# Performance work log

Hardware: AMD Instinct MI355X
Metric: run time of the kernel (lower is better)

The kernel has to match this reference:

```python
import jax, jax.numpy as jnp
import numpy as np
from jax import lax

H, P, N, G, K, CHUNK = 64, 64, 128, 1, 4, 256
D_MODEL = 2048
D_INNER = H * P            # 4096
CONV_DIM = D_INNER + 2 * G * N  # 4352
EPS = 1e-5


def setup_inputs() -> dict:
    key = jax.random.key(0)
    ks = jax.random.split(key, 6)
    s = lambda k, shape, scale: jax.random.normal(k, shape, jnp.float32) * scale
    return {
        "hidden_states": s(ks[0], (2, 2048, D_MODEL), 1.0),
        "in_proj_w": s(ks[1], (D_MODEL, D_INNER + CONV_DIM + H), D_MODEL ** -0.5),
        "conv_w": s(ks[2], (CONV_DIM, K), K ** -0.5),
        "conv_b": jnp.zeros((CONV_DIM,), jnp.float32),
        "dt_bias": jnp.ones((H,), jnp.float32),
        "A_log": jnp.log(jnp.arange(1, H + 1, dtype=jnp.float32)),
        "D_param": jnp.ones((H,), jnp.float32),
        "norm_w": jnp.ones((D_INNER,), jnp.float32),
        "out_proj_w": s(ks[3], (D_INNER, D_MODEL), D_INNER ** -0.5),
    }


def _mamba2_forward(hidden_states, in_proj_w, conv_w, conv_b, dt_bias, A_log, D_param, norm_w, out_proj_w):
    b, l, _ = hidden_states.shape
    c = l // CHUNK  # number of chunks

    # in_proj -> gate | conv channels (x,B,C) | dt
    proj = hidden_states @ in_proj_w
    gate = proj[..., :D_INNER]
    hbc = proj[..., D_INNER:D_INNER + CONV_DIM]
    dt = proj[..., D_INNER + CONV_DIM:]  # [b,l,H]

    # depthwise causal conv1d + silu
    xt = hbc.transpose(0, 2, 1)  # [b, CONV_DIM, l]
    y = lax.conv_general_dilated(
        xt, conv_w[:, None, :], window_strides=(1,), padding=[(K - 1, 0)],
        feature_group_count=CONV_DIM, dimension_numbers=("NCH", "OIH", "NCH"))
    hbc = jax.nn.silu(y + conv_b[None, :, None]).transpose(0, 2, 1)  # [b,l,CONV_DIM]

    # split into x / B / C per group (unflatten over groups as in torch code)
    per_g = D_INNER // G
    hg = hbc.reshape(b, l, G, per_g + 2 * N)
    x = hg[..., :per_g].reshape(b, l, H, P)                 # [b,l,h,p]
    Bm = hg[..., per_g:per_g + N]                            # [b,l,g,n]
    Cm = hg[..., per_g + N:]                                 # [b,l,g,n]
    hpg = H // G
    Bh = jnp.repeat(Bm, hpg, axis=2)                         # [b,l,h,n]
    Ch = jnp.repeat(Cm, hpg, axis=2)

    # dt: softplus(dt + bias), clamp per time_step_limit (0, inf)
    dt = jax.nn.softplus(dt + dt_bias)                       # [b,l,h]
    A = -jnp.exp(A_log)                                      # [h]

    # chunk the sequence
    x_c = x.reshape(b, c, CHUNK, H, P)
    B_c = Bh.reshape(b, c, CHUNK, H, N)
    C_c = Ch.reshape(b, c, CHUNK, H, N)
    dt_c = dt.reshape(b, c, CHUNK, H)

    dA = dt_c * A[None, None, None, :]                       # [b,c,L,h]
    cum = jnp.cumsum(dA, axis=2)                             # [b,c,L,h]

    # intra-chunk (diagonal block): decay[i,j] = exp(cum_i - cum_j), i>=j
    diff = cum[:, :, :, None, :] - cum[:, :, None, :, :]     # [b,c,i,j,h]
    i = jnp.arange(CHUNK)
    mask = i[:, None] >= i[None, :]
    decay = jnp.exp(jnp.where(mask[None, None, :, :, None], diff, -jnp.inf))
    scores = jnp.einsum("bcihn,bcjhn->bcijh", C_c, B_c) * decay * dt_c[:, :, None, :, :]
    Y_diag = jnp.einsum("bcijh,bcjhp->bcihp", scores, x_c)   # [b,c,L,h,p]

    # per-chunk final states
    decay_states = jnp.exp(cum[:, :, -1:, :] - cum)          # [b,c,L,h]
    states = jnp.einsum("bclh,bclhn,bclhp->bchpn", decay_states * dt_c, B_c, x_c)
    chunk_decay = jnp.exp(cum[:, :, -1, :])                  # [b,c,h]

    # inter-chunk recurrence over chunks
    def step(prev, inp):
        st, cd = inp  # [b,h,p,n], [b,h]
        new = cd[:, :, None, None] * prev + st
        return new, prev

    init = jnp.zeros((b, H, P, N), hidden_states.dtype)
    _, prev_states = lax.scan(step, init, (jnp.moveaxis(states, 1, 0), jnp.moveaxis(chunk_decay, 1, 0)))
    prev_states = jnp.moveaxis(prev_states, 0, 1)            # [b,c,h,p,n]

    state_decay_out = jnp.exp(cum)                           # [b,c,L,h]
    Y_off = jnp.einsum("bclhn,bchpn,bclh->bclhp", C_c, prev_states, state_decay_out)

    yh = (Y_diag + Y_off).reshape(b, l, H, P) + D_param[None, None, :, None] * x
    yr = yh.reshape(b, l, D_INNER)

    # gated RMSNorm
    hidden = yr * jax.nn.silu(gate)
    var = jnp.mean(hidden * hidden, axis=-1, keepdims=True)
    hidden = hidden * lax.rsqrt(var + EPS) * norm_w

    return hidden @ out_proj_w


def reference(hidden_states, in_proj_w, conv_w, conv_b, dt_bias, A_log, D_param, norm_w, out_proj_w):
    return _mamba2_forward(hidden_states, in_proj_w, conv_w, conv_b, dt_bias, A_log, D_param, norm_w, out_proj_w)
```

## Files before the change

kernel.cpp:

```cpp
#include <hip/hip_runtime.h>
#include <hip/hip_bf16.h>


typedef __attribute__((ext_vector_type(8))) _Float16 f16x8;
typedef __attribute__((ext_vector_type(4))) float f32x4;

#define GLD16(gp, lp) __builtin_amdgcn_global_load_lds( \
    (__attribute__((address_space(1))) void*)(gp),      \
    (__attribute__((address_space(3))) void*)(lp), 16, 0, 0)

__device__ __forceinline__ unsigned short f2h(float v) {
  _Float16 h = (_Float16)v;
  return *reinterpret_cast<unsigned short*>(&h);
}
__device__ __forceinline__ float h2f(unsigned short u) {
  _Float16 h = *reinterpret_cast<_Float16*>(&u);
  return (float)h;
}
__device__ __forceinline__ float siluf(float x) { return x / (1.f + expf(-x)); }

__global__ __launch_bounds__(256) void prep(const float* __restrict__ hs,
                                            const float* __restrict__ Win,
                                            _Float16* __restrict__ Ah,
                                            _Float16* __restrict__ WtH,
                                            float* __restrict__ zf) {
  __shared__ __attribute__((aligned(16))) char smemP[32768];
  const int bid = blockIdx.x;
  const int tid = threadIdx.x;
  if (bid < 1024) {
    float (*Xs)[2048] = reinterpret_cast<float (*)[2048]>(smemP);
    int t0 = bid * 4;
#pragma unroll
    for (int i = 0; i < 8; i++) {
      int e = tid * 4 + i * 1024;
      int tok = e >> 11, k = e & 2047;
      *reinterpret_cast<float4*>(&Xs[tok][k]) =
          *reinterpret_cast<const float4*>(&hs[(long)(t0 + tok) * 2048 + k]);
    }
    __syncthreads();
    int h = tid & 63, tg = tid >> 6;
    float a0 = 0.f, a1 = 0.f, a2 = 0.f, a3 = 0.f;
    const float* wcol = Win + 8448 + h;
    for (int k = 0; k < 2048; k += 4) {
      a0 = fmaf(Xs[tg][k + 0], wcol[(long)(k + 0) * 8512], a0);
      a1 = fmaf(Xs[tg][k + 1], wcol[(long)(k + 1) * 8512], a1);
      a2 = fmaf(Xs[tg][k + 2], wcol[(long)(k + 2) * 8512], a2);
      a3 = fmaf(Xs[tg][k + 3], wcol[(long)(k + 3) * 8512], a3);
    }
    zf[(long)(t0 + tg) * 64 + h] = (a0 + a1) + (a2 + a3);
  } else if (bid < 9216) {
    long i = ((long)(bid - 1024) * 256 + tid) * 4;
    float4 v = *reinterpret_cast<const float4*>(hs + i);
    ushort4 u;
    u.x = f2h(v.x); u.y = f2h(v.y); u.z = f2h(v.z); u.w = f2h(v.w);
    *reinterpret_cast<ushort4*>((unsigned short*)Ah + i) = u;
  } else {
    float (*tile)[33] = reinterpret_cast<float (*)[33]>(smemP);
    int i = bid - 9216;
    int c0 = (i % 264) * 32, r0 = (i / 264) * 32;
    int tx = tid & 31, ty = tid >> 5;
#pragma unroll
    for (int j = 0; j < 4; j++)
      tile[ty + j * 8][tx] = Win[(long)(r0 + ty + j * 8) * 8512 + c0 + tx];
    __syncthreads();
#pragma unroll
    for (int j = 0; j < 4; j++) {
      int c = c0 + ty + j * 8, r = r0 + tx;
      WtH[(long)c * 2048 + r] = (_Float16)tile[tx][ty + j * 8];
    }
  }
}

__global__ __launch_bounds__(512, 2) void gemm_in8(const _Float16* __restrict__ A,
                                                   const _Float16* __restrict__ Bt,
                                                   _Float16* __restrict__ gate,
                                                   float* __restrict__ hbcf,
                                                   float* __restrict__ rparts) {
  __shared__ __attribute__((aligned(128))) char ldsB[131072];
  const int tid = threadIdx.x;
  const int lane = tid & 63;
  const int wv = tid >> 6;
  const int wr = wv >> 2, wc = wv & 3;
  const int wg = blockIdx.x;
  const bool rem = wg >= 512;
  int by, bxn, kbase, zz;
  if (!rem) {
    const int xcd = wg & 7, j = wg >> 3;
    by = (xcd >> 2) * 8 + (j >> 3);
    bxn = (xcd & 3) * 8 + (j & 7);
    kbase = 0; zz = 0;
  } else {
    const int idx = wg - 512;
    by = idx & 15; zz = idx >> 4; bxn = 32; kbase = zz * 256;
  }

  const int srow = tid >> 3;
  const int scolg = (tid & 7) ^ (srow & 7);
  const _Float16* Ab = A + (long)by * 524288 + (long)srow * 2048 + scolg * 8 + kbase;
  const _Float16* Bb = Bt + (long)bxn * 524288 + (long)srow * 2048 + scolg * 8 + kbase;
  const int ldst = tid << 4;

#define STAGE_A(tau, h) do {                                              \
    const _Float16* g_ = Ab + (long)(h) * 262144 + (tau) * 64;            \
    char* l_ = ldsB + ((((tau) & 1) << 2) + (h)) * 16384 + ldst;          \
    GLD16(g_, l_); GLD16(g_ + 131072, l_ + 8192); } while (0)
#define STAGE_B(tau, h) do {                                              \
    const _Float16* g_ = Bb + (long)(h) * 262144 + (tau) * 64;            \
    char* l_ = ldsB + ((((tau) & 1) << 2) + 2 + (h)) * 16384 + ldst;      \
    GLD16(g_, l_); GLD16(g_ + 131072, l_ + 8192); } while (0)

  const int fr = lane & 15;
  const int c16 = (lane >> 4) ^ (fr & 7);
  const int aOff = wr * 16384 + fr * 128 + c16 * 16;
  const int bOff = (2 + (wc >> 1)) * 16384 + ((wc & 1) * 64 + fr) * 128 + c16 * 16;
#define RD_A(b, mi, k32) (*(const f16x8*)(ldsB + ((aOff + (b) * 65536 + (mi) * 2048) ^ ((k32) * 64))))
#define RD_B(b, ni, k32) (*(const f16x8*)(ldsB + ((bOff + (b) * 65536 + (ni) * 2048) ^ ((k32) * 64))))

#define BAR() __builtin_amdgcn_s_barrier()
#define WLG0() asm volatile("s_waitcnt lgkmcnt(0)" ::: "memory")
#define WLG8() asm volatile("s_waitcnt lgkmcnt(8)" ::: "memory")
#define WVM4() asm volatile("s_waitcnt vmcnt(4)" ::: "memory")

  f32x4 acc[8][4];
#pragma unroll
  for (int mi = 0; mi < 8; ++mi)
#pragma unroll
    for (int ni = 0; ni < 4; ++ni) acc[mi][ni] = f32x4{0.f, 0.f, 0.f, 0.f};

  STAGE_A(0, 0); STAGE_A(0, 1); STAGE_B(0, 0); STAGE_B(0, 1);
  STAGE_B(1, 0); STAGE_B(1, 1);
  WVM4(); BAR();

#define MFMA_Q(MI0, MI1, x0, x1, x2, x3, PB)                                        \
  __builtin_amdgcn_s_setprio(1);                                                    \
  _Pragma("unroll") for (int ni = 0; ni < 4; ++ni) {                                \
    acc[MI0][ni] = __builtin_amdgcn_mfma_f32_16x16x32_f16(x0, PB[ni][0], acc[MI0][ni], 0, 0, 0); \
    acc[MI0][ni] = __builtin_amdgcn_mfma_f32_16x16x32_f16(x1, PB[ni][1], acc[MI0][ni], 0, 0, 0); \
    acc[MI1][ni] = __builtin_amdgcn_mfma_f32_16x16x32_f16(x2, PB[ni][0], acc[MI1][ni], 0, 0, 0); \
    acc[MI1][ni] = __builtin_amdgcn_mfma_f32_16x16x32_f16(x3, PB[ni][1], acc[MI1][ni], 0, 0, 0); \
  }                                                                                 \
  __builtin_amdgcn_s_setprio(0);

#define ITER8(u, msk) do {                                                          \
    const int t1 = (2 * (u) + 1) & (msk);                                           \
    const int t2 = (2 * (u) + 2) & (msk);                                           \
    const int t3 = (2 * (u) + 3) & (msk);                                           \
    f16x8 PB0[4][2];                                                                \
    _Pragma("unroll") for (int ni = 0; ni < 4; ++ni) {                              \
      PB0[ni][0] = RD_B(0, ni, 0); PB0[ni][1] = RD_B(0, ni, 1); }                   \
    {                                                                               \
      f16x8 x0 = RD_A(0, 0, 0), x1 = RD_A(0, 0, 1), x2 = RD_A(0, 1, 0), x3 = RD_A(0, 1, 1); \
      STAGE_A(t1, 0); WLG8(); BAR(); WLG0();                                        \
      MFMA_Q(0, 1, x0, x1, x2, x3, PB0) BAR();                                      \
    }                                                                               \
    {                                                                               \
      f16x8 x0 = RD_A(0, 2, 0), x1 = RD_A(0, 2, 1), x2 = RD_A(0, 3, 0), x3 = RD_A(0, 3, 1); \
      STAGE_A(t1, 1); BAR(); WLG0();                                                \
      MFMA_Q(2, 3, x0, x1, x2, x3, PB0) BAR();                                      \
    }                                                                               \
    {                                                                               \
      f16x8 x0 = RD_A(0, 4, 0), x1 = RD_A(0, 4, 1), x2 = RD_A(0, 5, 0), x3 = RD_A(0, 5, 1); \
      STAGE_B(t2, 0); BAR(); WLG0();                                                \
      MFMA_Q(4, 5, x0, x1, x2, x3, PB0) BAR();                                      \
    }                                                                               \
    {                                                                               \
      f16x8 x0 = RD_A(0, 6, 0), x1 = RD_A(0, 6, 1), x2 = RD_A(0, 7, 0), x3 = RD_A(0, 7, 1); \
      STAGE_B(t2, 1); BAR(); WLG0();                                                \
      MFMA_Q(6, 7, x0, x1, x2, x3, PB0) WVM4(); BAR();                              \
    }                                                                               \
    f16x8 PB1[4][2];                                                                \
    _Pragma("unroll") for (int ni = 0; ni < 4; ++ni) {                              \
      PB1[ni][0] = RD_B(1, ni, 0); PB1[ni][1] = RD_B(1, ni, 1); }                   \
    {                                                                               \
      f16x8 x0 = RD_A(1, 0, 0), x1 = RD_A(1, 0, 1), x2 = RD_A(1, 1, 0), x3 = RD_A(1, 1, 1); \
      STAGE_A(t2, 0); WLG8(); BAR(); WLG0();                                        \
      MFMA_Q(0, 1, x0, x1, x2, x3, PB1) BAR();                                      \
    }                                                                               \
    {                                                                               \
      f16x8 x0 = RD_A(1, 2, 0), x1 = RD_A(1, 2, 1), x2 = RD_A(1, 3, 0), x3 = RD_A(1, 3, 1); \
      STAGE_A(t2, 1); BAR(); WLG0();                                                \
      MFMA_Q(2, 3, x0, x1, x2, x3, PB1) BAR();                                      \
    }                                                                               \
    {                                                                               \
      f16x8 x0 = RD_A(1, 4, 0), x1 = RD_A(1, 4, 1), x2 = RD_A(1, 5, 0), x3 = RD_A(1, 5, 1); \
      STAGE_B(t3, 0); BAR(); WLG0();                                                \
      MFMA_Q(4, 5, x0, x1, x2, x3, PB1) BAR();                                      \
    }                                                                               \
    {                                                                               \
      f16x8 x0 = RD_A(1, 6, 0), x1 = RD_A(1, 6, 1), x2 = RD_A(1, 7, 0), x3 = RD_A(1, 7, 1); \
      STAGE_B(t3, 1); BAR(); WLG0();                                                \
      MFMA_Q(6, 7, x0, x1, x2, x3, PB1) WVM4(); BAR();                              \
    }                                                                               \
  } while (0)

  if (!rem) {
    for (int u = 0; u < 16; ++u) ITER8(u, 31);
  } else {
    for (int u = 0; u < 2; ++u) ITER8(u, 3);
  }

  const int m0 = by * 256 + wr * 128;
  const int cl = lane & 15, rq = (lane >> 4) * 4;
  if (!rem) {
    const int n0 = bxn * 256 + wc * 64;
    if (bxn < 16) {
#pragma unroll
      for (int mi = 0; mi < 8; ++mi)
#pragma unroll
        for (int r = 0; r < 4; ++r) {
          long rowoff = (long)(m0 + mi * 16 + rq + r) * 4096 + n0 + cl;
#pragma unroll
          for (int ni = 0; ni < 4; ++ni) gate[rowoff + ni * 16] = (_Float16)acc[mi][ni][r];
        }
    } else {
#pragma unroll
      for (int mi = 0; mi < 8; ++mi)
#pragma unroll
        for (int r = 0; r < 4; ++r) {
          long rowoff = (long)(m0 + mi * 16 + rq + r) * 4352 + (n0 - 4096) + cl;
#pragma unroll
          for (int ni = 0; ni < 4; ++ni) hbcf[rowoff + ni * 16] = acc[mi][ni][r];
        }
    }
  } else {
    float* rp = rparts + (long)zz * 1048576;
    const int ncol = wc * 64;
#pragma unroll
    for (int mi = 0; mi < 8; ++mi)
#pragma unroll
      for (int r = 0; r < 4; ++r) {
        long rowoff = (long)(m0 + mi * 16 + rq + r) * 256 + ncol + cl;
#pragma unroll
        for (int ni = 0; ni < 4; ++ni) rp[rowoff + ni * 16] = acc[mi][ni][r];
      }
  }
#undef STAGE_A
#undef STAGE_B
#undef RD_A
#undef RD_B
#undef ITER8
}

__global__ __launch_bounds__(256) void fuse2(const float* __restrict__ zf,
                                             const float* __restrict__ dtb,
                                             const float* __restrict__ Alog,
                                             float* __restrict__ dt_f,
                                             float* __restrict__ cum_f,
                                             float* __restrict__ cuml,
                                             const float* __restrict__ rp,
                                             float* __restrict__ hbcf,
                                             const float* __restrict__ Wout,
                                             _Float16* __restrict__ WoutT) {
  __shared__ __attribute__((aligned(16))) char smem2[4352];
  const int bid = blockIdx.x;
  const int tid = threadIdx.x;
  if (bid < 16) {
    float (*segsum)[64] = reinterpret_cast<float (*)[64]>(smem2);
    int bc = bid;
    int h = tid & 63, seg = tid >> 6;
    int t0 = bc * 256;
    float Ah = -expf(Alog[h]);
    float bias = dtb[h];
    float s = 0.f;
    for (int j = 0; j < 64; j++) {
      int t = t0 + seg * 64 + j;
      float z = zf[(long)t * 64 + h] + bias;
      float v = (z > 20.f) ? z : log1pf(expf(z));
      dt_f[(long)t * 64 + h] = v;
      s += v * Ah;
    }
    segsum[seg][h] = s;
    __syncthreads();
    float run = 0.f;
    for (int k = 0; k < seg; k++) run += segsum[k][h];
    for (int j = 0; j < 64; j++) {
      int t = t0 + seg * 64 + j;
      run += dt_f[(long)t * 64 + h] * Ah;
      cum_f[(long)t * 64 + h] = run;
    }
    if (seg == 3) cuml[bc * 64 + h] = run;
  } else if (bid < 1040) {
    long e = ((long)(bid - 16) * 256 + tid) * 4;
    float4 s = *reinterpret_cast<const float4*>(rp + e);
#pragma unroll
    for (int z = 1; z < 8; ++z) {
      float4 v = *reinterpret_cast<const float4*>(rp + (long)z * 1048576 + e);
      s.x += v.x; s.y += v.y; s.z += v.z; s.w += v.w;
    }
    long row = e >> 8, col = e & 255;
    *reinterpret_cast<float4*>(hbcf + row * 4352 + 4096 + col) = s;
  } else {
    float (*tile)[33] = reinterpret_cast<float (*)[33]>(smem2);
    int i = bid - 1040;
    int c0 = (i & 63) * 32, r0 = (i >> 6) * 32;
    int tx = tid & 31, ty = tid >> 5;
#pragma unroll
    for (int j = 0; j < 4; j++)
      tile[ty + j * 8][tx] = Wout[(long)(r0 + ty + j * 8) * 2048 + c0 + tx];
    __syncthreads();
#pragma unroll
    for (int j = 0; j < 4; j++) {
      int c = c0 + ty + j * 8, r = r0 + tx;
      WoutT[(long)c * 4096 + r] = (_Float16)tile[tx][ty + j * 8];
    }
  }
}

__global__ __launch_bounds__(256) void convx(const float* __restrict__ hbcf,
                                             const float* __restrict__ convw,
                                             const float* __restrict__ convb,
                                             _Float16* __restrict__ x16,
                                             _Float16* __restrict__ B16,
                                             _Float16* __restrict__ C16,
                                             unsigned short* __restrict__ xT16) {
  __shared__ unsigned short tile[64][66];
  const int bx = blockIdx.x, t0 = blockIdx.y * 64;
  const int tid = threadIdx.x;
  const int tq = tid & 63, tg = tid >> 6;
  const int q0 = (bx < 64) ? bx * 64 : 4096 + (bx - 64) * 64;
  const int q = q0 + tq;
  const int ts = t0 + tg * 16;
  const int bstart = ts & ~2047;
  const float* colq = hbcf + q;
  float4 wq = *reinterpret_cast<const float4*>(convw + q * 4);
  float bconv = convb[q];
  float v3 = (ts - 3 >= bstart) ? colq[(long)(ts - 3) * 4352] : 0.f;
  float v2 = (ts - 2 >= bstart) ? colq[(long)(ts - 2) * 4352] : 0.f;
  float v1 = (ts - 1 >= bstart) ? colq[(long)(ts - 1) * 4352] : 0.f;
  if (bx < 64) {
#pragma unroll
    for (int j = 0; j < 16; ++j) {
      int t = ts + j;
      float v0 = colq[(long)t * 4352];
      float a = bconv + v3 * wq.x + v2 * wq.y + v1 * wq.z + v0 * wq.w;
      unsigned short o = f2h(siluf(a));
      ((unsigned short*)x16)[(long)t * 4096 + q] = o;
      tile[tg * 16 + j][tq] = o;
      v3 = v2; v2 = v1; v1 = v0;
    }
    __syncthreads();
    int tx = tid & 15, ty = tid >> 4;
#pragma unroll
    for (int i = 0; i < 4; ++i) {
      int c = ty + i * 16;
      ushort4 v;
      v.x = tile[4 * tx + 0][c]; v.y = tile[4 * tx + 1][c];
      v.z = tile[4 * tx + 2][c]; v.w = tile[4 * tx + 3][c];
      *(ushort4*)&xT16[(long)(q0 + c) * 4096 + t0 + 4 * tx] = v;
    }
  } else {
#pragma unroll
    for (int j = 0; j < 16; ++j) {
      int t = ts + j;
      float v0 = colq[(long)t * 4352];
      float a = bconv + v3 * wq.x + v2 * wq.y + v1 * wq.z + v0 * wq.w;
      _Float16 o = (_Float16)siluf(a);
      if (q < 4224) B16[(long)t * 128 + (q - 4096)] = o;
      else C16[(long)t * 128 + (q - 4224)] = o;
      v3 = v2; v2 = v1; v1 = v0;
    }
  }
}

__global__ __launch_bounds__(256) void fuse3(const unsigned short* __restrict__ xT16,
                                             const _Float16* __restrict__ B16,
                                             const _Float16* __restrict__ C16,
                                             const float* __restrict__ dt_f,
                                             const float* __restrict__ cum_f,
                                             const float* __restrict__ cuml,
                                             float* __restrict__ states,
                                             float* __restrict__ CBT) {
  __shared__ __attribute__((aligned(16))) char smem3[16384];
  const int bid = blockIdx.x;
  const int tid = threadIdx.x;
  const int wv = tid >> 6, lane = tid & 63;
  const int mr = lane & 15, koff = (lane >> 4) * 8;
  if (bid < 1024) {
    float* w_s = (float*)smem3;
    unsigned short* Aw = (unsigned short*)(smem3 + 1024);
    unsigned short* BT = (unsigned short*)(smem3 + 6144);
    int h = bid & 63, bc = bid >> 6;
    int t0 = bc * 256;
    {
      int t = t0 + tid;
      w_s[tid] = expf(cuml[bc * 64 + h] - cum_f[(long)t * 64 + h]) * dt_f[(long)t * 64 + h];
    }
    __syncthreads();
    f32x4 acc[4][2];
#pragma unroll
    for (int mi = 0; mi < 4; mi++)
#pragma unroll
      for (int nj = 0; nj < 2; nj++) acc[mi][nj] = f32x4{0.f, 0.f, 0.f, 0.f};
    for (int kt = 0; kt < 8; kt++) {
      {
        int p = tid >> 2, tq2 = tid & 3;
        const unsigned short* g = &xT16[((long)(h * 64 + p)) * 4096 + t0 + kt * 32 + tq2 * 8];
        ushort4 u0 = *(const ushort4*)g, u1 = *(const ushort4*)(g + 4);
        const float* wp = &w_s[kt * 32 + tq2 * 8];
        ushort4 o0, o1;
        o0.x = f2h(h2f(u0.x) * wp[0]); o0.y = f2h(h2f(u0.y) * wp[1]);
        o0.z = f2h(h2f(u0.z) * wp[2]); o0.w = f2h(h2f(u0.w) * wp[3]);
        o1.x = f2h(h2f(u1.x) * wp[4]); o1.y = f2h(h2f(u1.y) * wp[5]);
        o1.z = f2h(h2f(u1.z) * wp[6]); o1.w = f2h(h2f(u1.w) * wp[7]);
        *(ushort4*)&Aw[p * 40 + tq2 * 8] = o0;
        *(ushort4*)&Aw[p * 40 + tq2 * 8 + 4] = o1;
      }
      {
        int tl = tid >> 3, ng = tid & 7;
        const unsigned short* g = (const unsigned short*)B16 +
                                  ((long)(t0 + kt * 32 + tl)) * 128 + ng * 16;
#pragma unroll
        for (int j = 0; j < 16; j++) BT[(ng * 16 + j) * 40 + tl] = g[j];
      }
      __syncthreads();
      f16x8 af[4], bf[2];
#pragma unroll
      for (int mi = 0; mi < 4; mi++)
        af[mi] = *(const f16x8*)&Aw[(mi * 16 + mr) * 40 + koff];
#pragma unroll
      for (int nj = 0; nj < 2; nj++)
        bf[nj] = *(const f16x8*)&BT[((wv * 2 + nj) * 16 + mr) * 40 + koff];
#pragma unroll
      for (int mi = 0; mi < 4; mi++)
#pragma unroll
        for (int nj = 0; nj < 2; nj++)
          acc[mi][nj] = __builtin_amdgcn_mfma_f32_16x16x32_f16(af[mi], bf[nj],
                                                               acc[mi][nj], 0, 0, 0);
      __syncthreads();
    }
    int cl = lane & 15, rq = (lane >> 4) * 4;
    long base = ((long)(bc * 64 + h)) * 8192;
#pragma unroll
    for (int mi = 0; mi < 4; mi++)
#pragma unroll
      for (int r = 0; r < 4; r++) {
        int p = mi * 16 + rq + r;
#pragma unroll
        for (int nj = 0; nj < 2; nj++) {
          int n = (wv * 2 + nj) * 16 + cl;
          states[base + p * 128 + n] = acc[mi][nj][r];
        }
      }
  } else {
    _Float16* As = (_Float16*)smem3;
    _Float16* Bs = (_Float16*)(smem3 + 8192);
    int i = bid - 1024;
    int bx = i & 1, by = (i >> 1) & 1, bz = i >> 2;
    const _Float16* Ab = C16 + (long)bz * 32768 + (long)by * 128 * 128;
    const _Float16* Bb = B16 + (long)bz * 32768 + (long)bx * 128 * 128;
    const int c0 = wv * 128 + lane;
    const int c1 = c0 + 64;
    const long ra0 = (long)(c0 >> 2) * 128 + (c0 & 3) * 8;
    const long ra1 = (long)(c1 >> 2) * 128 + (c1 & 3) * 8;
    f32x4 acc[4][4];
#pragma unroll
    for (int mi = 0; mi < 4; mi++)
#pragma unroll
      for (int ni = 0; ni < 4; ni++) acc[mi][ni] = f32x4{0.f, 0.f, 0.f, 0.f};
    const int mrow = (wv & 1) * 64 + (lane & 15);
    const int nrow = (wv >> 1) * 64 + (lane & 15);
    for (int k0 = 0; k0 < 128; k0 += 32) {
      GLD16(Ab + ra0 + k0, (char*)As + c0 * 16);
      GLD16(Ab + ra1 + k0, (char*)As + c1 * 16);
      GLD16(Bb + ra0 + k0, (char*)Bs + c0 * 16);
      GLD16(Bb + ra1 + k0, (char*)Bs + c1 * 16);
      __syncthreads();
      f16x8 af[4], bfr[4];
#pragma unroll
      for (int mi = 0; mi < 4; mi++)
        af[mi] = *(const f16x8*)(As + (mrow + mi * 16) * 32 + koff);
#pragma unroll
      for (int ni = 0; ni < 4; ni++)
        bfr[ni] = *(const f16x8*)(Bs + (nrow + ni * 16) * 32 + koff);
#pragma unroll
      for (int mi = 0; mi < 4; mi++)
#pragma unroll
        for (int ni = 0; ni < 4; ni++)
          acc[mi][ni] = __builtin_amdgcn_mfma_f32_16x16x32_f16(af[mi], bfr[ni],
                                                               acc[mi][ni], 0, 0, 0);
      __syncthreads();
    }
    const int m0 = by * 128 + (wv & 1) * 64;
    const int n0 = bx * 128 + (wv >> 1) * 64;
    const int cl = lane & 15, rq = (lane >> 4) * 4;
    const long zc = (long)bz * 65536;
#pragma unroll
    for (int mi = 0; mi < 4; mi++)
#pragma unroll
      for (int r = 0; r < 4; r++) {
        long rowoff = zc + (long)(m0 + mi * 16 + rq + r) * 256 + n0 + cl;
#pragma unroll
        for (int ni = 0; ni < 4; ni++) CBT[rowoff + ni * 16] = acc[mi][ni][r];
      }
  }
}

__global__ __launch_bounds__(256) void recur_kernel(float* __restrict__ states,
                                                    const float* __restrict__ cuml) {
  int g = blockIdx.x;
  int bh = g >> 3, js = g & 7;
  int b = bh >> 6, h = bh & 63;
  int tid = threadIdx.x;
  float4 prev = make_float4(0.f, 0.f, 0.f, 0.f);
  for (int c = 0; c < 8; c++) {
    int bc = b * 8 + c;
    float cd = expf(cuml[bc * 64 + h]);
    long o = (long)(bc * 64 + h) * 8192 + js * 1024 + tid * 4;
    float4 st = *reinterpret_cast<const float4*>(&states[o]);
    *reinterpret_cast<float4*>(&states[o]) = prev;
    prev.x = fmaf(cd, prev.x, st.x);
    prev.y = fmaf(cd, prev.y, st.y);
    prev.z = fmaf(cd, prev.z, st.z);
    prev.w = fmaf(cd, prev.w, st.w);
  }
}

__global__ __launch_bounds__(256) void yfused(const unsigned short* __restrict__ xT16,
                                              const unsigned short* __restrict__ x16,
                                              const unsigned short* __restrict__ C16,
                                              const float* __restrict__ CBT,
                                              const float* __restrict__ states,
                                              const float* __restrict__ dt_f,
                                              const float* __restrict__ cum_f,
                                              const float* __restrict__ Dp,
                                              float* __restrict__ Ysum) {
  int h = blockIdx.x, bc = blockIdx.y;
  int t0 = bc * 256, tid = threadIdx.x;
  __shared__ unsigned short Sb[256 * 40];
  __shared__ unsigned short Xb[64 * 264];
  __shared__ float cum_s[256], dt_s[256];
  int i = tid;
  cum_s[i] = cum_f[(long)(t0 + i) * 64 + h];
  dt_s[i] = dt_f[(long)(t0 + i) * 64 + h];
  {
    int p = tid >> 2, tq = tid & 3;
    const unsigned short* g = &xT16[((long)(h * 64 + p)) * 4096 + t0 + tq * 64];
    unsigned short* l = &Xb[p * 264 + tq * 64];
#pragma unroll
    for (int c = 0; c < 8; c++)
      *(uint4*)(l + c * 8) = *(const uint4*)(g + c * 8);
  }
  __syncthreads();
  float cum_i = cum_s[i];
  const float* cbrow = CBT + (long)bc * 65536 + (long)i * 256;
  int wv = tid >> 6, lane = tid & 63;
  int mr = lane & 15, koff = (lane >> 4) * 8;
  f32x4 acc[4][4];
#pragma unroll
  for (int mi = 0; mi < 4; mi++)
#pragma unroll
    for (int ni = 0; ni < 4; ni++) acc[mi][ni] = f32x4{0.f, 0.f, 0.f, 0.f};
  for (int kt = 0; kt < 8; kt++) {
    int k0 = kt * 32;
#pragma unroll
    for (int c = 0; c < 8; c++) {
      float4 cb = *(const float4*)&cbrow[k0 + c * 4];
      ushort4 o;
      {
        int j = k0 + c * 4 + 0;
        float s = (j <= i) ? cb.x * expf(cum_i - cum_s[j]) * dt_s[j] : 0.f;
        o.x = f2h(s);
      }
      {
        int j = k0 + c * 4 + 1;
        float s = (j <= i) ? cb.y * expf(cum_i - cum_s[j]) * dt_s[j] : 0.f;
        o.y = f2h(s);
      }
      {
        int j = k0 + c * 4 + 2;
        float s = (j <= i) ? cb.z * expf(cum_i - cum_s[j]) * dt_s[j] : 0.f;
        o.z = f2h(s);
      }
      {
        int j = k0 + c * 4 + 3;
        float s = (j <= i) ? cb.w * expf(cum_i - cum_s[j]) * dt_s[j] : 0.f;
        o.w = f2h(s);
      }
      *(ushort4*)&Sb[i * 40 + c * 4] = o;
    }
    __syncthreads();
    if (kt <= 2 * wv + 1) {
      f16x8 af[4], bf[4];
#pragma unroll
      for (int mi = 0; mi < 4; mi++)
        af[mi] = *(const f16x8*)&Sb[(64 * wv + mi * 16 + mr) * 40 + koff];
#pragma unroll
      for (int ni = 0; ni < 4; ni++)
        bf[ni] = *(const f16x8*)&Xb[(ni * 16 + mr) * 264 + k0 + koff];
#pragma unroll
      for (int mi = 0; mi < 4; mi++)
#pragma unroll
        for (int ni = 0; ni < 4; ni++)
          acc[mi][ni] = __builtin_amdgcn_mfma_f32_16x16x32_f16(af[mi], bf[ni],
                                                               acc[mi][ni], 0, 0, 0);
    }
    __syncthreads();
  }
  {
    int p = tid >> 2, nq = tid & 3;
    const float* g = &states[((long)(bc * 64 + h)) * 8192 + p * 128 + nq * 32];
    unsigned short* l = &Xb[p * 136 + nq * 32];
#pragma unroll
    for (int c = 0; c < 8; c++) {
      float4 v = *(const float4*)(g + c * 4);
      ushort4 u;
      u.x = f2h(v.x); u.y = f2h(v.y); u.z = f2h(v.z); u.w = f2h(v.w);
      *(ushort4*)(l + c * 4) = u;
    }
  }
  float fac_i = expf(cum_i);
  for (int kn = 0; kn < 4; kn++) {
    {
      const unsigned short* g = &C16[((long)(t0 + i)) * 128 + kn * 32];
#pragma unroll
      for (int c = 0; c < 8; c++) {
        ushort4 u = *(const ushort4*)(g + c * 4);
        ushort4 o;
        o.x = f2h(h2f(u.x) * fac_i); o.y = f2h(h2f(u.y) * fac_i);
        o.z = f2h(h2f(u.z) * fac_i); o.w = f2h(h2f(u.w) * fac_i);
        *(ushort4*)&Sb[i * 40 + c * 4] = o;
      }
    }
    __syncthreads();
    f16x8 af[4], bf[4];
#pragma unroll
    for (int mi = 0; mi < 4; mi++)
      af[mi] = *(const f16x8*)&Sb[(64 * wv + mi * 16 + mr) * 40 + koff];
#pragma unroll
    for (int ni = 0; ni < 4; ni++)
      bf[ni] = *(const f16x8*)&Xb[(ni * 16 + mr) * 136 + kn * 32 + koff];
#pragma unroll
    for (int mi = 0; mi < 4; mi++)
#pragma unroll
      for (int ni = 0; ni < 4; ni++)
        acc[mi][ni] = __builtin_amdgcn_mfma_f32_16x16x32_f16(af[mi], bf[ni],
                                                             acc[mi][ni], 0, 0, 0);
    __syncthreads();
  }
  float Dh = Dp[h];
  int cl = lane & 15, rq = (lane >> 4) * 4;
#pragma unroll
  for (int mi = 0; mi < 4; mi++)
#pragma unroll
    for (int r = 0; r < 4; r++) {
      long row = t0 + 64 * wv + mi * 16 + rq + r;
      float* yr = &Ysum[row * 4096 + h * 64];
      const unsigned short* xr = &x16[row * 4096 + h * 64];
#pragma unroll
      for (int ni = 0; ni < 4; ni++) {
        int p = ni * 16 + cl;
        yr[p] = acc[mi][ni][r] + Dh * h2f(xr[p]);
      }
    }
}

__global__ __launch_bounds__(256) void norm_kernel(const float* __restrict__ Ysum,
                                                   const _Float16* __restrict__ gate,
                                                   const float* __restrict__ nw,
                                                   _Float16* __restrict__ hid) {
  int t = blockIdx.x;
  int tid = threadIdx.x;
  float hv[16];
  float ss = 0.f;
#pragma unroll
  for (int k = 0; k < 4; k++) {
    int d = tid * 4 + k * 1024;
    float4 y = *reinterpret_cast<const float4*>(&Ysum[(long)t * 4096 + d]);
    ushort4 gu = *reinterpret_cast<const ushort4*>(gate + (long)t * 4096 + d);
    float h0 = y.x * siluf(h2f(gu.x)), h1 = y.y * siluf(h2f(gu.y));
    float h2 = y.z * siluf(h2f(gu.z)), h3 = y.w * siluf(h2f(gu.w));
    hv[k * 4 + 0] = h0; hv[k * 4 + 1] = h1; hv[k * 4 + 2] = h2; hv[k * 4 + 3] = h3;
    ss += h0 * h0 + h1 * h1 + h2 * h2 + h3 * h3;
  }
#pragma unroll
  for (int o = 32; o > 0; o >>= 1) ss += __shfl_down(ss, o, 64);
  __shared__ float ws4[4];
  if ((tid & 63) == 0) ws4[tid >> 6] = ss;
  __syncthreads();
  float var = (ws4[0] + ws4[1] + ws4[2] + ws4[3]) * (1.f / 4096.f);
  float scale = rsqrtf(var + 1e-5f);
#pragma unroll
  for (int k = 0; k < 4; k++) {
    int d = tid * 4 + k * 1024;
    ushort4 u;
#pragma unroll
    for (int c = 0; c < 4; c++)
      ((unsigned short*)&u)[c] = f2h(hv[k * 4 + c] * scale * nw[d + c]);
    *reinterpret_cast<ushort4*>(hid + (long)t * 4096 + d) = u;
  }
}

__global__ __launch_bounds__(512, 2) void gemm_out8(const _Float16* __restrict__ A,
                                                    const _Float16* __restrict__ Bt,
                                                    float* __restrict__ Cp) {
  __shared__ __attribute__((aligned(128))) char ldsB[131072];
  const int tid = threadIdx.x;
  const int lane = tid & 63;
  const int wv = tid >> 6;
  const int wr = wv >> 2, wc = wv & 3;
  const int wg = blockIdx.x;
  const int xcd = wg & 7, j = wg >> 3;
  const int z = j >> 4, t = j & 15;
  const int by = (xcd >> 1) * 4 + (t >> 2);
  const int bx = (xcd & 1) * 4 + (t & 3);

  const int srow = tid >> 3;
  const int scolg = (tid & 7) ^ (srow & 7);
  const _Float16* Ab = A + (long)by * 256 * 4096 + (long)z * 2048 +
                       (long)srow * 4096 + scolg * 8;
  const _Float16* Bb = Bt + (long)bx * 256 * 4096 + (long)z * 2048 +
                       (long)srow * 4096 + scolg * 8;
  const int ldst = tid << 4;

#define STAGE_A(tau, h) do {                                              \
    const _Float16* g_ = Ab + (long)(h) * 524288 + (tau) * 64;            \
    char* l_ = ldsB + ((((tau) & 1) << 2) + (h)) * 16384 + ldst;          \
    GLD16(g_, l_); GLD16(g_ + 262144, l_ + 8192); } while (0)
#define STAGE_B(tau, h) do {                                              \
    const _Float16* g_ = Bb + (long)(h) * 524288 + (tau) * 64;            \
    char* l_ = ldsB + ((((tau) & 1) << 2) + 2 + (h)) * 16384 + ldst;      \
    GLD16(g_, l_); GLD16(g_ + 262144, l_ + 8192); } while (0)

  const int fr = lane & 15;
  const int c16 = (lane >> 4) ^ (fr & 7);
  const int aOff = wr * 16384 + fr * 128 + c16 * 16;
  const int bOff = (2 + (wc >> 1)) * 16384 + ((wc & 1) * 64 + fr) * 128 + c16 * 16;
#define RD_A(b, mi, k32) (*(const f16x8*)(ldsB + ((aOff + (b) * 65536 + (mi) * 2048) ^ ((k32) * 64))))
#define RD_B(b, ni, k32) (*(const f16x8*)(ldsB + ((bOff + (b) * 65536 + (ni) * 2048) ^ ((k32) * 64))))

  f32x4 acc[8][4];
#pragma unroll
  for (int mi = 0; mi < 8; ++mi)
#pragma unroll
    for (int ni = 0; ni < 4; ++ni) acc[mi][ni] = f32x4{0.f, 0.f, 0.f, 0.f};

  STAGE_A(0, 0); STAGE_A(0, 1); STAGE_B(0, 0); STAGE_B(0, 1);
  STAGE_B(1, 0); STAGE_B(1, 1);
  WVM4(); BAR();

  for (int u = 0; u < 16; ++u) {
    const int t1 = 2 * u + 1;
    const int t2 = (2 * u + 2) & 31;
    const int t3 = (2 * u + 3) & 31;
    f16x8 PB0[4][2];
#pragma unroll
    for (int ni = 0; ni < 4; ++ni) { PB0[ni][0] = RD_B(0, ni, 0); PB0[ni][1] = RD_B(0, ni, 1); }
    {
      f16x8 x0 = RD_A(0, 0, 0), x1 = RD_A(0, 0, 1), x2 = RD_A(0, 1, 0), x3 = RD_A(0, 1, 1);
      STAGE_A(t1, 0); WLG8(); BAR(); WLG0();
      MFMA_Q(0, 1, x0, x1, x2, x3, PB0) BAR();
    }
    {
      f16x8 x0 = RD_A(0, 2, 0), x1 = RD_A(0, 2, 1), x2 = RD_A(0, 3, 0), x3 = RD_A(0, 3, 1);
      STAGE_A(t1, 1); BAR(); WLG0();
      MFMA_Q(2, 3, x0, x1, x2, x3, PB0) BAR();
    }
    {
      f16x8 x0 = RD_A(0, 4, 0), x1 = RD_A(0, 4, 1), x2 = RD_A(0, 5, 0), x3 = RD_A(0, 5, 1);
      STAGE_B(t2, 0); BAR(); WLG0();
      MFMA_Q(4, 5, x0, x1, x2, x3, PB0) BAR();
    }
    {
      f16x8 x0 = RD_A(0, 6, 0), x1 = RD_A(0, 6, 1), x2 = RD_A(0, 7, 0), x3 = RD_A(0, 7, 1);
      STAGE_B(t2, 1); BAR(); WLG0();
      MFMA_Q(6, 7, x0, x1, x2, x3, PB0) WVM4(); BAR();
    }
    f16x8 PB1[4][2];
#pragma unroll
    for (int ni = 0; ni < 4; ++ni) { PB1[ni][0] = RD_B(1, ni, 0); PB1[ni][1] = RD_B(1, ni, 1); }
    {
      f16x8 x0 = RD_A(1, 0, 0), x1 = RD_A(1, 0, 1), x2 = RD_A(1, 1, 0), x3 = RD_A(1, 1, 1);
      STAGE_A(t2, 0); WLG8(); BAR(); WLG0();
      MFMA_Q(0, 1, x0, x1, x2, x3, PB1) BAR();
    }
    {
      f16x8 x0 = RD_A(1, 2, 0), x1 = RD_A(1, 2, 1), x2 = RD_A(1, 3, 0), x3 = RD_A(1, 3, 1);
      STAGE_A(t2, 1); BAR(); WLG0();
      MFMA_Q(2, 3, x0, x1, x2, x3, PB1) BAR();
    }
    {
      f16x8 x0 = RD_A(1, 4, 0), x1 = RD_A(1, 4, 1), x2 = RD_A(1, 5, 0), x3 = RD_A(1, 5, 1);
      STAGE_B(t3, 0); BAR(); WLG0();
      MFMA_Q(4, 5, x0, x1, x2, x3, PB1) BAR();
    }
    {
      f16x8 x0 = RD_A(1, 6, 0), x1 = RD_A(1, 6, 1), x2 = RD_A(1, 7, 0), x3 = RD_A(1, 7, 1);
      STAGE_B(t3, 1); BAR(); WLG0();
      MFMA_Q(6, 7, x0, x1, x2, x3, PB1) WVM4(); BAR();
    }
  }
  const int m0 = by * 256 + wr * 128;
  const int n0 = bx * 256 + wc * 64;
  const int cl = lane & 15, rq = (lane >> 4) * 4;
  float* Cb = Cp + (long)z * 8388608;
#pragma unroll
  for (int mi = 0; mi < 8; ++mi)
#pragma unroll
    for (int r = 0; r < 4; ++r) {
      long rowoff = (long)(m0 + mi * 16 + rq + r) * 2048 + n0 + cl;
#pragma unroll
      for (int ni = 0; ni < 4; ++ni) Cb[rowoff + ni * 16] = acc[mi][ni][r];
    }
#undef STAGE_A
#undef STAGE_B
#undef RD_A
#undef RD_B
#undef BAR
#undef WLG0
#undef WLG8
#undef WVM4
#undef MFMA_Q
}

__global__ __launch_bounds__(256) void add_out(const float* __restrict__ p,
                                               float* __restrict__ o) {
  long i = ((long)blockIdx.x * 256 + threadIdx.x) * 4;
  float4 a = *reinterpret_cast<const float4*>(p + i);
  float4 b = *reinterpret_cast<const float4*>(p + 8388608 + i);
  float4 r;
  r.x = a.x + b.x; r.y = a.y + b.y; r.z = a.z + b.z; r.w = a.w + b.w;
  *reinterpret_cast<float4*>(o + i) = r;
}

extern "C" void kernel_launch(void* const* d_in, const int* in_sizes, int n_in,
                              void* d_out, int out_size, void* d_ws, size_t ws_size,
                              hipStream_t stream) {
  (void)in_sizes; (void)n_in; (void)out_size; (void)ws_size;
  const float* hs    = (const float*)d_in[0];
  const float* Win   = (const float*)d_in[1];
  const float* convw = (const float*)d_in[2];
  const float* convb = (const float*)d_in[3];
  const float* dtb   = (const float*)d_in[4];
  const float* Alog  = (const float*)d_in[5];
  const float* Dp    = (const float*)d_in[6];
  const float* nw    = (const float*)d_in[7];
  const float* Wout  = (const float*)d_in[8];
  float* out = (float*)d_out;

  char* base = (char*)d_ws;
  size_t off = 0;
  auto take = [&](size_t n) { char* r = base + off; off += (n + 255) & ~(size_t)255; return r; };
  float*    hbcf  = (float*)take(4096UL * 4352 * 4);
  _Float16* gateh = (_Float16*)take(4096UL * 4096 * 2);
  _Float16* Ah    = (_Float16*)take(4096UL * 2048 * 2);
  _Float16* WtH   = (_Float16*)take(8448UL * 2048 * 2);
  _Float16* xT16  = (_Float16*)take(4096UL * 4096 * 2);
  _Float16* B16   = (_Float16*)take(4096UL * 128 * 2);
  _Float16* C16   = (_Float16*)take(4096UL * 128 * 2);
  float*    zf    = (float*)take(4096UL * 64 * 4);
  float*    dt_f  = (float*)take(4096UL * 64 * 4);
  float*    cum_f = (float*)take(4096UL * 64 * 4);
  float*    cuml  = (float*)take(16UL * 64 * 4);
  float*    CBT   = (float*)take(16UL * 256 * 256 * 4);
  float*    states= (float*)take(1024UL * 8192 * 4);
  float*    Ysum  = hbcf;
  float*    oparts= hbcf;
  float*    rparts= states;
  _Float16* WoutT = Ah;
  _Float16* x16   = WtH;
  _Float16* hid   = (_Float16*)states;

  prep<<<26112, 256, 0, stream>>>(hs, Win, Ah, WtH, zf);
  gemm_in8<<<dim3(640), 512, 0, stream>>>(Ah, WtH, gateh, hbcf, rparts);
  fuse2<<<9232, 256, 0, stream>>>(zf, dtb, Alog, dt_f, cum_f, cuml,
                                  rparts, hbcf, Wout, WoutT);
  convx<<<dim3(68, 64), 256, 0, stream>>>(hbcf, convw, convb, x16, B16, C16,
                                          (unsigned short*)xT16);
  fuse3<<<1088, 256, 0, stream>>>((const unsigned short*)xT16, B16, C16,
                                  dt_f, cum_f, cuml, states, CBT);
  recur_kernel<<<1024, 256, 0, stream>>>(states, cuml);
  yfused<<<dim3(64, 16), 256, 0, stream>>>((const unsigned short*)xT16,
                                           (const unsigned short*)x16,
                                           (const unsigned short*)C16,
                                           CBT, states, dt_f, cum_f, Dp, Ysum);
  norm_kernel<<<4096, 256, 0, stream>>>(Ysum, gateh, nw, hid);
  gemm_out8<<<dim3(256), 512, 0, stream>>>(hid, WoutT, oparts);
  add_out<<<8192, 256, 0, stream>>>(oparts, out);
}
```

Measured before the change: 695.2 us.

## Fuse gating and sum-of-squares into yfused; replace norm with in-place scale

The gated SiLU multiply and the per-row sum of squares move into the yfused epilogue. It writes fp16 gated hidden directly and accumulates row sums with atomics into a buffer that fuse3 zeroes. A light scale kernel then applies rsqrt and norm_w in place. This removes the fp32 Ysum round trip. The LDS read address computation in the GEMMs also changes from an XOR to a select between two precomputed offsets, and the output partial buffers are reassigned. The atomics add contention, and the sum order is now nondeterministic.

```diff
diff --git a/kernel.cpp b/kernel.cpp
--- a/kernel.cpp
+++ b/kernel.cpp
@@ -111,10 +111,12 @@
 
   const int fr = lane & 15;
   const int c16 = (lane >> 4) ^ (fr & 7);
-  const int aOff = wr * 16384 + fr * 128 + c16 * 16;
-  const int bOff = (2 + (wc >> 1)) * 16384 + ((wc & 1) * 64 + fr) * 128 + c16 * 16;
-#define RD_A(b, mi, k32) (*(const f16x8*)(ldsB + ((aOff + (b) * 65536 + (mi) * 2048) ^ ((k32) * 64))))
-#define RD_B(b, ni, k32) (*(const f16x8*)(ldsB + ((bOff + (b) * 65536 + (ni) * 2048) ^ ((k32) * 64))))
+  const int aOff0 = wr * 16384 + fr * 128 + c16 * 16;
+  const int aOff1 = aOff0 ^ 64;
+  const int bOff0 = (2 + (wc >> 1)) * 16384 + ((wc & 1) * 64 + fr) * 128 + c16 * 16;
+  const int bOff1 = bOff0 ^ 64;
+#define RD_A(b, mi, k32) (*(const f16x8*)(ldsB + ((k32) ? aOff1 : aOff0) + (b) * 65536 + (mi) * 2048))
+#define RD_B(b, ni, k32) (*(const f16x8*)(ldsB + ((k32) ? bOff1 : bOff0) + (b) * 65536 + (ni) * 2048))
 
 #define BAR() __builtin_amdgcn_s_barrier()
 #define WLG0() asm volatile("s_waitcnt lgkmcnt(0)" ::: "memory")
@@ -369,7 +371,8 @@
                                              const float* __restrict__ cum_f,
                                              const float* __restrict__ cuml,
                                              float* __restrict__ states,
-                                             float* __restrict__ CBT) {
+                                             float* __restrict__ CBT,
+                                             float* __restrict__ ssq) {
   __shared__ __attribute__((aligned(16))) char smem3[16384];
   const int bid = blockIdx.x;
   const int tid = threadIdx.x;
@@ -441,7 +444,7 @@
           states[base + p * 128 + n] = acc[mi][nj][r];
         }
       }
-  } else {
+  } else if (bid < 1088) {
     _Float16* As = (_Float16*)smem3;
     _Float16* Bs = (_Float16*)(smem3 + 8192);
     int i = bid - 1024;
@@ -492,6 +495,9 @@
 #pragma unroll
         for (int ni = 0; ni < 4; ni++) CBT[rowoff + ni * 16] = acc[mi][ni][r];
       }
+  } else {
+    int i = (bid - 1088) * 1024 + tid * 4;
+    *reinterpret_cast<float4*>(&ssq[i]) = make_float4(0.f, 0.f, 0.f, 0.f);
   }
 }
 
@@ -518,12 +524,14 @@
 __global__ __launch_bounds__(256) void yfused(const unsigned short* __restrict__ xT16,
                                               const unsigned short* __restrict__ x16,
                                               const unsigned short* __restrict__ C16,
+                                              const unsigned short* __restrict__ gate,
                                               const float* __restrict__ CBT,
                                               const float* __restrict__ states,
                                               const float* __restrict__ dt_f,
                                               const float* __restrict__ cum_f,
                                               const float* __restrict__ Dp,
-                                              float* __restrict__ Ysum) {
+                                              unsigned short* __restrict__ hid,
+                                              float* __restrict__ ssq) {
   int h = blockIdx.x, bc = blockIdx.y;
   int t0 = bc * 256, tid = threadIdx.x;
   __shared__ unsigned short Sb[256 * 40];
@@ -644,55 +652,49 @@
 #pragma unroll
     for (int r = 0; r < 4; r++) {
       long row = t0 + 64 * wv + mi * 16 + rq + r;
-      float* yr = &Ysum[row * 4096 + h * 64];
       const unsigned short* xr = &x16[row * 4096 + h * 64];
+      const unsigned short* gr = &gate[row * 4096 + h * 64];
+      unsigned short* hw = &hid[row * 4096 + h * 64];
+      float ssp = 0.f;
 #pragma unroll
       for (int ni = 0; ni < 4; ni++) {
         int p = ni * 16 + cl;
-        yr[p] = acc[mi][ni][r] + Dh * h2f(xr[p]);
-      }
-    }
-}
-
-__global__ __launch_bounds__(256) void norm_kernel(const float* __restrict__ Ysum,
-                                                   const _Float16* __restrict__ gate,
-                                                   const float* __restrict__ nw,
-                                                   _Float16* __restrict__ hid) {
-  int t = blockIdx.x;
+        float yv = acc[mi][ni][r] + Dh * h2f(xr[p]);
+        float hv = yv * siluf(h2f(gr[p]));
+        hw[p] = f2h(hv);
+        ssp += hv * hv;
+      }
+#pragma unroll
+      for (int o = 8; o > 0; o >>= 1) ssp += __shfl_down(ssp, o, 16);
+      if (cl == 0) atomicAdd(&ssq[row], ssp);
+    }
+}
+
+__global__ __launch_bounds__(256) void scale_kernel(const float* __restrict__ ssq,
+                                                    const float* __restrict__ nw,
+                                                    unsigned short* __restrict__ hid) {
+  int row = blockIdx.x;
   int tid = threadIdx.x;
-  float hv[16];
-  float ss = 0.f;
-#pragma unroll
-  for (int k = 0; k < 4; k++) {
-    int d = tid * 4 + k * 1024;
-    float4 y = *reinterpret_cast<const float4*>(&Ysum[(long)t * 4096 + d]);
-    ushort4 gu = *reinterpret_cast<const ushort4*>(gate + (long)t * 4096 + d);
-    float h0 = y.x * siluf(h2f(gu.x)), h1 = y.y * siluf(h2f(gu.y));
-    float h2 = y.z * siluf(h2f(gu.z)), h3 = y.w * siluf(h2f(gu.w));
-    hv[k * 4 + 0] = h0; hv[k * 4 + 1] = h1; hv[k * 4 + 2] = h2; hv[k * 4 + 3] = h3;
-    ss += h0 * h0 + h1 * h1 + h2 * h2 + h3 * h3;
-  }
-#pragma unroll
-  for (int o = 32; o > 0; o >>= 1) ss += __shfl_down(ss, o, 64);
-  __shared__ float ws4[4];
-  if ((tid & 63) == 0) ws4[tid >> 6] = ss;
-  __syncthreads();
-  float var = (ws4[0] + ws4[1] + ws4[2] + ws4[3]) * (1.f / 4096.f);
-  float scale = rsqrtf(var + 1e-5f);
-#pragma unroll
-  for (int k = 0; k < 4; k++) {
-    int d = tid * 4 + k * 1024;
-    ushort4 u;
-#pragma unroll
-    for (int c = 0; c < 4; c++)
-      ((unsigned short*)&u)[c] = f2h(hv[k * 4 + c] * scale * nw[d + c]);
-    *reinterpret_cast<ushort4*>(hid + (long)t * 4096 + d) = u;
+  float sc = rsqrtf(ssq[row] * (1.f / 4096.f) + 1e-5f);
+  unsigned short* hp = hid + (long)row * 4096;
+  int d0 = tid * 16;
+#pragma unroll
+  for (int c = 0; c < 4; c++) {
+    int d = d0 + c * 4;
+    ushort4 u = *reinterpret_cast<ushort4*>(&hp[d]);
+    float4 w = *reinterpret_cast<const float4*>(&nw[d]);
+    u.x = f2h(h2f(u.x) * sc * w.x);
+    u.y = f2h(h2f(u.y) * sc * w.y);
+    u.z = f2h(h2f(u.z) * sc * w.z);
+    u.w = f2h(h2f(u.w) * sc * w.w);
+    *reinterpret_cast<ushort4*>(&hp[d]) = u;
   }
 }
 
 __global__ __launch_bounds__(512, 2) void gemm_out8(const _Float16* __restrict__ A,
                                                     const _Float16* __restrict__ Bt,
-                                                    float* __restrict__ Cp) {
+                                                    float* __restrict__ Cp0,
+                                                    float* __restrict__ Cp1) {
   __shared__ __attribute__((aligned(128))) char ldsB[131072];
   const int tid = threadIdx.x;
   const int lane = tid & 63;
@@ -723,10 +725,12 @@
 
   const int fr = lane & 15;
   const int c16 = (lane >> 4) ^ (fr & 7);
-  const int aOff = wr * 16384 + fr * 128 + c16 * 16;
-  const int bOff = (2 + (wc >> 1)) * 16384 + ((wc & 1) * 64 + fr) * 128 + c16 * 16;
-#define RD_A(b, mi, k32) (*(const f16x8*)(ldsB + ((aOff + (b) * 65536 + (mi) * 2048) ^ ((k32) * 64))))
-#define RD_B(b, ni, k32) (*(const f16x8*)(ldsB + ((bOff + (b) * 65536 + (ni) * 2048) ^ ((k32) * 64))))
+  const int aOff0 = wr * 16384 + fr * 128 + c16 * 16;
+  const int aOff1 = aOff0 ^ 64;
+  const int bOff0 = (2 + (wc >> 1)) * 16384 + ((wc & 1) * 64 + fr) * 128 + c16 * 16;
+  const int bOff1 = bOff0 ^ 64;
+#define RD_A(b, mi, k32) (*(const f16x8*)(ldsB + ((k32) ? aOff1 : aOff0) + (b) * 65536 + (mi) * 2048))
+#define RD_B(b, ni, k32) (*(const f16x8*)(ldsB + ((k32) ? bOff1 : bOff0) + (b) * 65536 + (ni) * 2048))
 
   f32x4 acc[8][4];
 #pragma unroll
@@ -792,7 +796,7 @@
   const int m0 = by * 256 + wr * 128;
   const int n0 = bx * 256 + wc * 64;
   const int cl = lane & 15, rq = (lane >> 4) * 4;
-  float* Cb = Cp + (long)z * 8388608;
+  float* Cb = z ? Cp1 : Cp0;
 #pragma unroll
   for (int mi = 0; mi < 8; ++mi)
 #pragma unroll
@@ -812,11 +816,12 @@
 #undef MFMA_Q
 }
 
-__global__ __launch_bounds__(256) void add_out(const float* __restrict__ p,
+__global__ __launch_bounds__(256) void add_out(const float* __restrict__ p0,
+                                               const float* __restrict__ p1,
                                                float* __restrict__ o) {
   long i = ((long)blockIdx.x * 256 + threadIdx.x) * 4;
-  float4 a = *reinterpret_cast<const float4*>(p + i);
-  float4 b = *reinterpret_cast<const float4*>(p + 8388608 + i);
+  float4 a = *reinterpret_cast<const float4*>(p0 + i);
+  float4 b = *reinterpret_cast<const float4*>(p1 + i);
   float4 r;
   r.x = a.x + b.x; r.y = a.y + b.y; r.z = a.z + b.z; r.w = a.w + b.w;
   *reinterpret_cast<float4*>(o + i) = r;
@@ -851,14 +856,15 @@
   float*    dt_f  = (float*)take(4096UL * 64 * 4);
   float*    cum_f = (float*)take(4096UL * 64 * 4);
   float*    cuml  = (float*)take(16UL * 64 * 4);
+  float*    ssq   = (float*)take(4096UL * 4);
   float*    CBT   = (float*)take(16UL * 256 * 256 * 4);
   float*    states= (float*)take(1024UL * 8192 * 4);
-  float*    Ysum  = hbcf;
-  float*    oparts= hbcf;
-  float*    rparts= states;
-  _Float16* WoutT = Ah;
-  _Float16* x16   = WtH;
-  _Float16* hid   = (_Float16*)states;
+  float*    rparts = states;
+  _Float16* WoutT  = Ah;
+  _Float16* x16    = WtH;
+  unsigned short* hid = (unsigned short*)hbcf;
+  float*    oparts0 = states;
+  float*    oparts1 = (float*)gateh;
 
   prep<<<26112, 256, 0, stream>>>(hs, Win, Ah, WtH, zf);
   gemm_in8<<<dim3(640), 512, 0, stream>>>(Ah, WtH, gateh, hbcf, rparts);
@@ -866,14 +872,17 @@
                                   rparts, hbcf, Wout, WoutT);
   convx<<<dim3(68, 64), 256, 0, stream>>>(hbcf, convw, convb, x16, B16, C16,
                                           (unsigned short*)xT16);
-  fuse3<<<1088, 256, 0, stream>>>((const unsigned short*)xT16, B16, C16,
-                                  dt_f, cum_f, cuml, states, CBT);
+  fuse3<<<1092, 256, 0, stream>>>((const unsigned short*)xT16, B16, C16,
+                                  dt_f, cum_f, cuml, states, CBT, ssq);
   recur_kernel<<<1024, 256, 0, stream>>>(states, cuml);
   yfused<<<dim3(64, 16), 256, 0, stream>>>((const unsigned short*)xT16,
                                            (const unsigned short*)x16,
                                            (const unsigned short*)C16,
-                                           CBT, states, dt_f, cum_f, Dp, Ysum);
-  norm_kernel<<<4096, 256, 0, stream>>>(Ysum, gateh, nw, hid);
-  gemm_out8<<<dim3(256), 512, 0, stream>>>(hid, WoutT, oparts);
-  add_out<<<8192, 256, 0, stream>>>(oparts, out);
-}
+                                           (const unsigned short*)gateh,
+                                           CBT, states, dt_f, cum_f, Dp,
+                                           hid, ssq);
+  scale_kernel<<<4096, 256, 0, stream>>>(ssq, nw, hid);
+  gemm_out8<<<dim3(256), 512, 0, stream>>>((const _Float16*)hid, WoutT,
+                                           oparts0, oparts1);
+  add_out<<<8192, 256, 0, stream>>>(oparts0, oparts1, out);
+}
```

After: 709.4 us. +2.0%, slower.
